# Optimization experiments

Measured on AMD Instinct MI355X. Metric: run time of the kernel, lower is better.

## Reference

```python
import jax, jax.numpy as jnp
import numpy as np

LN_EPS = 1e-3   # keras LayerNormalization default epsilon
STAB = 1e-3     # performer relu-kernel numerical stabilizer
N = 2           # number of blocks per branch


def layer_norm(x, g, b):
    m = jnp.mean(x, axis=-1, keepdims=True)
    v = jnp.mean(jnp.square(x - m), axis=-1, keepdims=True)
    return (x - m) * jax.lax.rsqrt(v + LN_EPS) * g + b


def favor(q_in, kv_in, Wq, Wk, Wv, Wo):
    # Performer FAVOR attention, relu kernel features (google-research fast_attention,
    # projection_matrix_type=None). q/k/v head projections have no bias.
    q = jnp.einsum('bld,dhm->blhm', q_in, Wq)
    k = jnp.einsum('bsd,dhm->bshm', kv_in, Wk)
    v = jnp.einsum('bsd,dhm->bshm', kv_in, Wv)
    norm = q.shape[-1] ** -0.25  # 1/sqrt(sqrt(head_dim))
    qp = jax.nn.relu(q * norm) + STAB
    kp = jax.nn.relu(k * norm) + STAB
    kv = jnp.einsum('bshm,bshd->bhmd', kp, v)
    num = jnp.einsum('blhm,bhmd->blhd', qp, kv)
    den = jnp.einsum('blhm,bhm->blh', qp, kp.sum(axis=1))
    out = num / den[..., None]
    return jnp.einsum('blhd,hde->ble', out, Wo)


def forward(obj_inputs, road_inputs,
            rg_dense_W, rg_dense_b, rg_qkv_W, rg_qkv_b,
            rg_Wq, rg_Wk, rg_Wv, rg_Wo, rg_ln_g, rg_ln_b, rg_fc_W, rg_fc_b,
            rg_out_W, rg_out_b,
            dense_W, dense_b, pos_emb,
            Wq, Wk, Wv, Wo, ln_g, ln_b, fc_W, fc_b):
    rgH = rg_dense_W.shape[1]
    # ---- roadgraph branch: performer self-attention blocks ----
    x = jax.nn.relu(road_inputs @ rg_dense_W + rg_dense_b)
    for i in range(N):
        qkv = jax.nn.relu(x @ rg_qkv_W + rg_qkv_b)
        q = qkv[..., :rgH]  # k,v splits unused by FastSelfAttention (it re-projects q)
        attn = favor(q, q, rg_Wq[i], rg_Wk[i], rg_Wv[i], rg_Wo[i])
        n = layer_norm(attn + x, rg_ln_g[i], rg_ln_b[i])
        y = jax.nn.relu(n @ rg_fc_W[i] + rg_fc_b[i])
        x = layer_norm(n + y, rg_ln_g[i], rg_ln_b[i])  # original reuses ln_block_1
    rg_out = jax.nn.relu(x @ rg_out_W + rg_out_b)
    # ---- object branch: performer cross-attention blocks ----
    x = jax.nn.relu(obj_inputs @ dense_W + dense_b)
    x = x + pos_emb  # learned position embedding, [T, H]
    for i in range(N):
        attn = favor(x, rg_out, Wq[i], Wk[i], Wv[i], Wo[i])
        n = layer_norm(attn + x, ln_g[i], ln_b[i])
        y = jax.nn.relu(n @ fc_W[i] + fc_b[i])
        x = layer_norm(n + y, ln_g[i], ln_b[i])  # original reuses ln_block_1
    return x


def setup_inputs() -> dict:
    B, T, V = 8, 128, 512
    S, F = 8192, 8
    rgH, H = 16, 1024
    rh, rd = 4, 4     # rg heads, head_dim
    h, d = 16, 64     # cross heads, head_dim
    keys = iter(jax.random.split(jax.random.key(0), 64))
    def rnd(shape, scale=1.0):
        return jax.random.normal(next(keys), shape, dtype=jnp.float32) * scale
    return {
        'obj_inputs': rnd((B, T, V)),
        'road_inputs': rnd((B, S, F)),
        'rg_dense_W': rnd((F, rgH), F ** -0.5), 'rg_dense_b': jnp.zeros((rgH,), jnp.float32),
        'rg_qkv_W': rnd((rgH, 3 * rgH), rgH ** -0.5), 'rg_qkv_b': jnp.zeros((3 * rgH,), jnp.float32),
        'rg_Wq': rnd((N, rgH, rh, rd), rgH ** -0.5),
        'rg_Wk': rnd((N, rgH, rh, rd), rgH ** -0.5),
        'rg_Wv': rnd((N, rgH, rh, rd), rgH ** -0.5),
        'rg_Wo': rnd((N, rh, rd, rgH), rgH ** -0.5),
        'rg_ln_g': jnp.ones((N, rgH), jnp.float32), 'rg_ln_b': jnp.zeros((N, rgH), jnp.float32),
        'rg_fc_W': rnd((N, rgH, rgH), rgH ** -0.5), 'rg_fc_b': jnp.zeros((N, rgH), jnp.float32),
        'rg_out_W': rnd((rgH, H), rgH ** -0.5), 'rg_out_b': jnp.zeros((H,), jnp.float32),
        'dense_W': rnd((V, H), V ** -0.5), 'dense_b': jnp.zeros((H,), jnp.float32),
        'pos_emb': rnd((T, H), 0.02),
        'Wq': rnd((N, H, h, d), H ** -0.5),
        'Wk': rnd((N, H, h, d), H ** -0.5),
        'Wv': rnd((N, H, h, d), H ** -0.5),
        'Wo': rnd((N, h, d, H), H ** -0.5),
        'ln_g': jnp.ones((N, H), jnp.float32), 'ln_b': jnp.zeros((N, H), jnp.float32),
        'fc_W': rnd((N, H, H), H ** -0.5), 'fc_b': jnp.zeros((N, H), jnp.float32),
    }


def reference(obj_inputs, road_inputs, rg_dense_W, rg_dense_b, rg_qkv_W, rg_qkv_b,
              rg_Wq, rg_Wk, rg_Wv, rg_Wo, rg_ln_g, rg_ln_b, rg_fc_W, rg_fc_b,
              rg_out_W, rg_out_b, dense_W, dense_b, pos_emb,
              Wq, Wk, Wv, Wo, ln_g, ln_b, fc_W, fc_b):
    return forward(obj_inputs, road_inputs, rg_dense_W, rg_dense_b, rg_qkv_W, rg_qkv_b,
                   rg_Wq, rg_Wk, rg_Wv, rg_Wo, rg_ln_g, rg_ln_b, rg_fc_W, rg_fc_b,
                   rg_out_W, rg_out_b, dense_W, dense_b, pos_emb,
                   Wq, Wk, Wv, Wo, ln_g, ln_b, fc_W, fc_b)
```

## Files before the change

### kernel.cpp

```cpp
#include <hip/hip_runtime.h>

typedef unsigned short u16;
typedef unsigned int u32;

using s8v = __attribute__((ext_vector_type(8))) short;
using f4v = __attribute__((ext_vector_type(4))) float;

#define LN_EPS 0.001f
#define STAB 0.001f
#define NORM_OBJ 0.35355339059327373f
#define NORM_ROAD 0.7071067811865476f

__device__ __forceinline__ float bf2f(u16 v) { return __uint_as_float(((u32)v) << 16); }
__device__ __forceinline__ u16 f2bf(float f) {
  u32 u = __float_as_uint(f);
  u32 r = (u + 0x7fffu + ((u >> 16) & 1u)) >> 16;
  return (u16)r;
}
__device__ __forceinline__ f4v mfma16(s8v a, s8v b, f4v c) {
  return __builtin_amdgcn_mfma_f32_16x16x32_bf16(a, b, c, 0, 0, 0);
}
__device__ __forceinline__ void ldsload16(void* lds, const void* g) {
  __builtin_amdgcn_global_load_lds((const __attribute__((address_space(1))) u32*)g,
                                   (__attribute__((address_space(3))) u32*)lds, 16, 0, 0);
}

struct TPair { const float* s; u16* d; };
struct TP11 { TPair p[11]; };

__global__ __launch_bounds__(256) void transpose_kernel(TP11 ps, int K, int N) {
  const float* __restrict__ src = ps.p[blockIdx.z].s;
  u16* __restrict__ dst = ps.p[blockIdx.z].d;
  int n0 = blockIdx.x * 64, k0 = blockIdx.y * 64;
  int t = threadIdx.x;
  __shared__ __align__(16) u16 lt[64 * 72];
#pragma unroll
  for (int j = 0; j < 4; ++j) {
    int p = t + 256 * j;
    int r = p >> 4, cb = p & 15;
    float4 v = *(const float4*)(src + (size_t)(k0 + r) * N + n0 + cb * 4);
    lt[r * 72 + cb * 4 + 0] = f2bf(v.x);
    lt[r * 72 + cb * 4 + 1] = f2bf(v.y);
    lt[r * 72 + cb * 4 + 2] = f2bf(v.z);
    lt[r * 72 + cb * 4 + 3] = f2bf(v.w);
  }
  __syncthreads();
#pragma unroll
  for (int j = 0; j < 2; ++j) {
    int q = t + 256 * j;
    int on = q >> 3, ocb = q & 7;
    u16 e[8];
#pragma unroll
    for (int i = 0; i < 8; ++i) e[i] = lt[(ocb * 8 + i) * 72 + on];
    uint4 v;
    v.x = (u32)e[0] | ((u32)e[1] << 16);
    v.y = (u32)e[2] | ((u32)e[3] << 16);
    v.z = (u32)e[4] | ((u32)e[5] << 16);
    v.w = (u32)e[6] | ((u32)e[7] << 16);
    *(uint4*)(dst + (size_t)(n0 + on) * K + k0 + ocb * 8) = v;
  }
}

__global__ __launch_bounds__(256) void cvt_kernel(const float* __restrict__ src,
                                                  u16* __restrict__ dst) {
  int i = (blockIdx.x * 256 + threadIdx.x) * 4;
  float4 v = *(const float4*)(src + i);
  uint2 o;
  o.x = (u32)f2bf(v.x) | ((u32)f2bf(v.y) << 16);
  o.y = (u32)f2bf(v.z) | ((u32)f2bf(v.w) << 16);
  *(uint2*)(dst + i) = o;
}

__global__ __launch_bounds__(256) void r0_kernel(const float* __restrict__ road,
    const float* __restrict__ W, const float* __restrict__ bias, float* __restrict__ x) {
  int row = blockIdx.x * 256 + threadIdx.x;
  float in[8];
  float4 v0 = *(const float4*)(road + (size_t)row * 8);
  float4 v1 = *(const float4*)(road + (size_t)row * 8 + 4);
  in[0] = v0.x; in[1] = v0.y; in[2] = v0.z; in[3] = v0.w;
  in[4] = v1.x; in[5] = v1.y; in[6] = v1.z; in[7] = v1.w;
#pragma unroll
  for (int j = 0; j < 16; ++j) {
    float s = bias[j];
#pragma unroll
    for (int c = 0; c < 8; ++c) s += in[c] * W[c * 16 + j];
    x[(size_t)row * 16 + j] = fmaxf(s, 0.f);
  }
}

__global__ __launch_bounds__(256) void ra_kernel(const float* __restrict__ x,
    const float* __restrict__ qkvW, const float* __restrict__ qkvb,
    const float* __restrict__ Wk, const float* __restrict__ Wv,
    float* __restrict__ kvr, float* __restrict__ ksr) {
  int t = threadIdx.x;
  int row = blockIdx.x * 256 + t;
  int b = row >> 13;
  float xv[16];
#pragma unroll
  for (int e = 0; e < 16; ++e) xv[e] = x[(size_t)row * 16 + e];
  float q16[16];
#pragma unroll
  for (int j = 0; j < 16; ++j) {
    float s = qkvb[j];
#pragma unroll
    for (int c = 0; c < 16; ++c) s += xv[c] * qkvW[c * 48 + j];
    q16[j] = fmaxf(s, 0.f);
  }
  float kp[16], vh[16];
#pragma unroll
  for (int hm = 0; hm < 16; ++hm) {
    float sk = 0.f, sv = 0.f;
#pragma unroll
    for (int c = 0; c < 16; ++c) {
      float q = q16[c];
      sk += q * Wk[c * 16 + hm];
      sv += q * Wv[c * 16 + hm];
    }
    kp[hm] = fmaxf(sk * NORM_ROAD, 0.f) + STAB;
    vh[hm] = sv;
  }
  __shared__ float l[80];
  if (t < 80) l[t] = 0.f;
  __syncthreads();
#pragma unroll
  for (int h = 0; h < 4; ++h)
#pragma unroll
    for (int m = 0; m < 4; ++m) {
      float kpv = kp[h * 4 + m];
      atomicAdd(&l[64 + h * 4 + m], kpv);
#pragma unroll
      for (int d = 0; d < 4; ++d) atomicAdd(&l[h * 16 + m * 4 + d], kpv * vh[h * 4 + d]);
    }
  __syncthreads();
  if (t < 64) atomicAdd(&kvr[b * 64 + t], l[t]);
  else if (t < 80) atomicAdd(&ksr[b * 16 + (t - 64)], l[t]);
}

__device__ __forceinline__ void ln16(const float* tv, const float* g, const float* bb, float* o) {
  float m = 0.f;
#pragma unroll
  for (int e = 0; e < 16; ++e) m += tv[e];
  m *= (1.f / 16.f);
  float var = 0.f;
#pragma unroll
  for (int e = 0; e < 16; ++e) { float d = tv[e] - m; var += d * d; }
  var *= (1.f / 16.f);
  float rstd = rsqrtf(var + LN_EPS);
#pragma unroll
  for (int e = 0; e < 16; ++e) o[e] = (tv[e] - m) * rstd * g[e] + bb[e];
}

__global__ __launch_bounds__(256) void rb_kernel(float* __restrict__ x,
    const float* __restrict__ qkvW, const float* __restrict__ qkvb,
    const float* __restrict__ Wq, const float* __restrict__ Wo,
    const float* __restrict__ lng, const float* __restrict__ lnb,
    const float* __restrict__ fcW, const float* __restrict__ fcb,
    const float* __restrict__ kvr, const float* __restrict__ ksr) {
  int row = blockIdx.x * 256 + threadIdx.x;
  int b = row >> 13;
  float xv[16];
#pragma unroll
  for (int e = 0; e < 16; ++e) xv[e] = x[(size_t)row * 16 + e];
  float q16[16];
#pragma unroll
  for (int j = 0; j < 16; ++j) {
    float s = qkvb[j];
#pragma unroll
    for (int c = 0; c < 16; ++c) s += xv[c] * qkvW[c * 48 + j];
    q16[j] = fmaxf(s, 0.f);
  }
  float qp[16];
#pragma unroll
  for (int hm = 0; hm < 16; ++hm) {
    float s = 0.f;
#pragma unroll
    for (int c = 0; c < 16; ++c) s += q16[c] * Wq[c * 16 + hm];
    qp[hm] = fmaxf(s * NORM_ROAD, 0.f) + STAB;
  }
  float attn[16];
#pragma unroll
  for (int e = 0; e < 16; ++e) attn[e] = 0.f;
#pragma unroll
  for (int h = 0; h < 4; ++h) {
    float den = 0.f;
#pragma unroll
    for (int m = 0; m < 4; ++m) den += qp[h * 4 + m] * ksr[b * 16 + h * 4 + m];
    float od[4];
#pragma unroll
    for (int d = 0; d < 4; ++d) {
      float num = 0.f;
#pragma unroll
      for (int m = 0; m < 4; ++m) num += qp[h * 4 + m] * kvr[b * 64 + h * 16 + m * 4 + d];
      od[d] = num / den;
    }
#pragma unroll
    for (int d = 0; d < 4; ++d)
#pragma unroll
      for (int e = 0; e < 16; ++e) attn[e] += od[d] * Wo[(h * 4 + d) * 16 + e];
  }
  float tv[16], n[16], o2[16];
#pragma unroll
  for (int e = 0; e < 16; ++e) tv[e] = attn[e] + xv[e];
  ln16(tv, lng, lnb, n);
#pragma unroll
  for (int j = 0; j < 16; ++j) {
    float s = fcb[j];
#pragma unroll
    for (int e = 0; e < 16; ++e) s += n[e] * fcW[e * 16 + j];
    tv[j] = n[j] + fmaxf(s, 0.f);
  }
  ln16(tv, lng, lnb, o2);
#pragma unroll
  for (int e = 0; e < 16; ++e) x[(size_t)row * 16 + e] = o2[e];
}

__global__ __launch_bounds__(256) void rc_kernel(const float* __restrict__ x,
    const float* __restrict__ W, const float* __restrict__ bias, u16* __restrict__ out) {
  const int t = threadIdx.x;
  const int cg = t & 63, rg = t >> 6;
  const int c0 = blockIdx.x * 256 + cg * 4;
  const int r0 = blockIdx.y * 16;
  __shared__ float lx[256];
  lx[t] = x[(size_t)(r0 + (t >> 4)) * 16 + (t & 15)];
  __syncthreads();
  float4 wv[16];
#pragma unroll
  for (int c = 0; c < 16; ++c) wv[c] = *(const float4*)(W + (size_t)c * 1024 + c0);
  float4 bv = *(const float4*)(bias + c0);
#pragma unroll
  for (int k = 0; k < 4; ++k) {
    int rr = rg * 4 + k;
    float s0 = bv.x, s1 = bv.y, s2 = bv.z, s3 = bv.w;
#pragma unroll
    for (int c = 0; c < 16; ++c) {
      float xv = lx[rr * 16 + c];
      s0 += xv * wv[c].x; s1 += xv * wv[c].y; s2 += xv * wv[c].z; s3 += xv * wv[c].w;
    }
    uint2 o;
    o.x = (u32)f2bf(fmaxf(s0, 0.f)) | ((u32)f2bf(fmaxf(s1, 0.f)) << 16);
    o.y = (u32)f2bf(fmaxf(s2, 0.f)) | ((u32)f2bf(fmaxf(s3, 0.f)) << 16);
    *(uint2*)(out + (size_t)(r0 + rr) * 1024 + c0) = o;
  }
}

__global__ __launch_bounds__(256) void gemm_kernel(
    const u16* __restrict__ A, const u16* __restrict__ BT, int K,
    float* __restrict__ outF, u16* __restrict__ outB,
    const float* __restrict__ bias, const float* __restrict__ resF, int resmod,
    float scale, int do_relu, float post) {
  const int n0 = blockIdx.x * 128, m0 = blockIdx.y * 128;
  const int t = threadIdx.x;
  const int wid = t >> 6, lane = t & 63, quad = lane >> 4, m16 = lane & 15;
  const int wm = wid >> 1, wn = wid & 1;
  const int lrr = lane >> 3;
  const int lcs = (((lane & 7) ^ lrr) * 8);
  const int sw = m16 & 7;
  __shared__ __align__(16) u16 smem[2 * 128 * 64];
  u16* Al = smem;
  u16* Bl = smem + 128 * 64;
  f4v acc[4][4];
#pragma unroll
  for (int i = 0; i < 4; ++i)
#pragma unroll
    for (int j = 0; j < 4; ++j) acc[i][j] = {0.f, 0.f, 0.f, 0.f};

  for (int kc = 0; kc < K; kc += 64) {
    __syncthreads();
#pragma unroll
    for (int j = 0; j < 4; ++j) {
      int rbase = wid * 32 + j * 8;
      ldsload16(Al + rbase * 64, A + (size_t)(m0 + rbase + lrr) * K + kc + lcs);
      ldsload16(Bl + rbase * 64, BT + (size_t)(n0 + rbase + lrr) * K + kc + lcs);
    }
    __syncthreads();
#pragma unroll
    for (int ko = 0; ko < 64; ko += 32) {
      int g0 = ko >> 3;
      s8v af[4], bfr[4];
#pragma unroll
      for (int tm = 0; tm < 4; ++tm)
        af[tm] = *(const s8v*)(Al + (wm * 64 + tm * 16 + m16) * 64 + ((g0 + quad) ^ sw) * 8);
#pragma unroll
      for (int tn = 0; tn < 4; ++tn)
        bfr[tn] = *(const s8v*)(Bl + (wn * 64 + tn * 16 + m16) * 64 + ((g0 + quad) ^ sw) * 8);
#pragma unroll
      for (int tm = 0; tm < 4; ++tm)
#pragma unroll
        for (int tn = 0; tn < 4; ++tn)
          acc[tm][tn] = mfma16(af[tm], bfr[tn], acc[tm][tn]);
    }
  }
#pragma unroll
  for (int tm = 0; tm < 4; ++tm)
#pragma unroll
    for (int tn = 0; tn < 4; ++tn)
#pragma unroll
      for (int r = 0; r < 4; ++r) {
        int row = m0 + wm * 64 + tm * 16 + quad * 4 + r;
        int col = n0 + wn * 64 + tn * 16 + m16;
        float v = acc[tm][tn][r] * scale;
        if (bias) v += bias[col];
        if (do_relu) v = fmaxf(v, 0.f);
        v += post;
        if (resF) v += resF[(size_t)(row % resmod) * 1024 + col];
        if (outF) outF[(size_t)row * 1024 + col] = v;
        if (outB) outB[(size_t)row * 1024 + col] = f2bf(v);
      }
}

__global__ __launch_bounds__(256) void kv_kernel(
    const u16* __restrict__ rgout,
    const u16* __restrict__ WkT0, const u16* __restrict__ WvT0,
    const u16* __restrict__ WkT1, const u16* __restrict__ WvT1,
    float* __restrict__ kv, float* __restrict__ ksum) {
  const int mt = blockIdx.x, h2 = blockIdx.y, b = blockIdx.z;
  const int lay = h2 >> 4, h = h2 & 15;
  const u16* __restrict__ WkT = lay ? WkT1 : WkT0;
  const u16* __restrict__ WvT = lay ? WvT1 : WvT0;
  kv += (size_t)lay * 524288;
  ksum += (size_t)lay * 8192;
  const int t = threadIdx.x;
  const int wid = t >> 6, lane = t & 63, quad = lane >> 4, m16 = lane & 15;
  const int wm = wid >> 1, wn = wid & 1;
  const int lrr = lane >> 3;
  const int lcs = (((lane & 7) ^ lrr) * 8);
  const int sw = m16 & 7;
  __shared__ __align__(16) u16 smem[2 * 128 * 72];
  u16* Al = smem;
  u16* Bl = smem + 128 * 64;
  const size_t abase = ((size_t)b * 8192 + (size_t)mt * 128) * 1024;
  f4v acc[4][4];
#pragma unroll
  for (int i = 0; i < 4; ++i)
#pragma unroll
    for (int j = 0; j < 4; ++j) acc[i][j] = {0.f, 0.f, 0.f, 0.f};

  for (int kc = 0; kc < 1024; kc += 64) {
    __syncthreads();
#pragma unroll
    for (int j = 0; j < 4; ++j) {
      int rbase = wid * 32 + j * 8;
      int r = rbase + lrr;
      ldsload16(Al + rbase * 64, rgout + abase + (size_t)r * 1024 + kc + lcs);
      const u16* bsrc = (r < 64) ? (WkT + (size_t)(h * 64 + r) * 1024)
                                 : (WvT + (size_t)(h * 64 + (r - 64)) * 1024);
      ldsload16(Bl + rbase * 64, bsrc + kc + lcs);
    }
    __syncthreads();
#pragma unroll
    for (int ko = 0; ko < 64; ko += 32) {
      int g0 = ko >> 3;
      s8v af[4], bfr[4];
#pragma unroll
      for (int tm = 0; tm < 4; ++tm)
        af[tm] = *(const s8v*)(Al + (wm * 64 + tm * 16 + m16) * 64 + ((g0 + quad) ^ sw) * 8);
#pragma unroll
      for (int tn = 0; tn < 4; ++tn)
        bfr[tn] = *(const s8v*)(Bl + (wn * 64 + tn * 16 + m16) * 64 + ((g0 + quad) ^ sw) * 8);
#pragma unroll
      for (int tm = 0; tm < 4; ++tm)
#pragma unroll
        for (int tn = 0; tn < 4; ++tn)
          acc[tm][tn] = mfma16(af[tm], bfr[tn], acc[tm][tn]);
    }
  }
  __syncthreads();
  u16* KPT = smem;
  u16* VT = smem + 64 * 136;
  {
    u16* dst = wn ? VT : KPT;
    const int sbase = wm * 64 + quad * 4;
#pragma unroll
    for (int tm = 0; tm < 4; ++tm)
#pragma unroll
      for (int tn = 0; tn < 4; ++tn) {
        float v0 = acc[tm][tn][0], v1 = acc[tm][tn][1];
        float v2 = acc[tm][tn][2], v3 = acc[tm][tn][3];
        if (wn == 0) {
          v0 = fmaxf(v0 * NORM_OBJ, 0.f) + STAB;
          v1 = fmaxf(v1 * NORM_OBJ, 0.f) + STAB;
          v2 = fmaxf(v2 * NORM_OBJ, 0.f) + STAB;
          v3 = fmaxf(v3 * NORM_OBJ, 0.f) + STAB;
        }
        uint2 o;
        o.x = (u32)f2bf(v0) | ((u32)f2bf(v1) << 16);
        o.y = (u32)f2bf(v2) | ((u32)f2bf(v3) << 16);
        int feat = tn * 16 + m16;
        *(uint2*)(dst + feat * 136 + sbase + tm * 16) = o;
      }
  }
  __syncthreads();
  if (t < 64) {
    float s = 0.f;
#pragma unroll
    for (int i = 0; i < 128; i += 8) {
      uint4 v = *(const uint4*)(KPT + t * 136 + i);
      u32 a[4] = {v.x, v.y, v.z, v.w};
#pragma unroll
      for (int q = 0; q < 4; ++q) {
        s += __uint_as_float(a[q] << 16);
        s += __uint_as_float(a[q] & 0xffff0000u);
      }
    }
    atomicAdd(&ksum[(size_t)(b * 16 + h) * 64 + t], s);
  }
  f4v a2[4];
#pragma unroll
  for (int tn = 0; tn < 4; ++tn) a2[tn] = {0.f, 0.f, 0.f, 0.f};
#pragma unroll
  for (int ks = 0; ks < 128; ks += 32) {
    s8v af = *(const s8v*)(KPT + (wid * 16 + m16) * 136 + ks + quad * 8);
#pragma unroll
    for (int tn = 0; tn < 4; ++tn) {
      s8v bv = *(const s8v*)(VT + (tn * 16 + m16) * 136 + ks + quad * 8);
      a2[tn] = mfma16(af, bv, a2[tn]);
    }
  }
#pragma unroll
  for (int tn = 0; tn < 4; ++tn)
#pragma unroll
    for (int r = 0; r < 4; ++r) {
      int m = wid * 16 + quad * 4 + r;
      int d = tn * 16 + m16;
      atomicAdd(&kv[((size_t)(b * 16 + h) * 64 + m) * 64 + d], a2[tn][r]);
    }
}

__global__ __launch_bounds__(256) void q2_kernel(const u16* __restrict__ qp,
    const float* __restrict__ kv, const float* __restrict__ ks, u16* __restrict__ out) {
  int wid = threadIdx.x >> 6, lane = threadIdx.x & 63;
  int row = blockIdx.x * 4 + wid;
  int b = row >> 7;
  int h0 = blockIdx.y * 4;
  for (int h = h0; h < h0 + 4; ++h) {
    const float* kvp = kv + (size_t)((b * 16 + h) * 64) * 64;
    const float* ksp = ks + (size_t)(b * 16 + h) * 64;
    const u16* qpp = qp + (size_t)row * 1024 + h * 64;
    float num = 0.f, den = 0.f;
    for (int m = 0; m < 64; ++m) {
      float qv = bf2f(qpp[m]);
      num += qv * kvp[m * 64 + lane];
      den += qv * ksp[m];
    }
    out[(size_t)row * 1024 + h * 64 + lane] = f2bf(num / den);
  }
}

__global__ __launch_bounds__(256) void ln_kernel(const float* __restrict__ in,
    const float* __restrict__ g, const float* __restrict__ bb,
    float* __restrict__ outF, u16* __restrict__ outB) {
  int row = blockIdx.x, t = threadIdx.x;
  const float* x = in + (size_t)row * 1024;
  float v[4];
  float s = 0.f, ss = 0.f;
#pragma unroll
  for (int j = 0; j < 4; ++j) {
    v[j] = x[t + 256 * j];
    s += v[j];
    ss += v[j] * v[j];
  }
  __shared__ float rs[256], rss[256];
  rs[t] = s; rss[t] = ss;
  __syncthreads();
  for (int o = 128; o > 0; o >>= 1) {
    if (t < o) { rs[t] += rs[t + o]; rss[t] += rss[t + o]; }
    __syncthreads();
  }
  float mean = rs[0] * (1.f / 1024.f);
  float var = rss[0] * (1.f / 1024.f) - mean * mean;
  float rstd = rsqrtf(var + LN_EPS);
#pragma unroll
  for (int j = 0; j < 4; ++j) {
    int c = t + 256 * j;
    float o = (v[j] - mean) * rstd * g[c] + bb[c];
    if (outF) outF[(size_t)row * 1024 + c] = o;
    if (outB) outB[(size_t)row * 1024 + c] = f2bf(o);
  }
}

static constexpr size_t MBy = 1048576;
static constexpr size_t OFF_XROAD = 0;
static constexpr size_t OFF_RGOUT = 4 * MBy;
static constexpr size_t OFF_KVR = OFF_RGOUT + 128 * MBy;
static constexpr size_t OFF_KSR = OFF_KVR + 2048;
static constexpr size_t OFF_KVO = OFF_KVR + 4096;
static constexpr size_t OFF_KSO = OFF_KVO + 4 * MBy;
static constexpr size_t OFF_WT = OFF_KSO + 65536;
static constexpr size_t OFF_XOBJ = OFF_WT + 21 * MBy;
static constexpr size_t OFF_XOBJB = OFF_XOBJ + 4 * MBy;
static constexpr size_t OFF_QP = OFF_XOBJB + 2 * MBy;
static constexpr size_t OFF_FOUT = OFF_QP + 2 * MBy;
static constexpr size_t OFF_T1 = OFF_FOUT + 2 * MBy;
static constexpr size_t OFF_N = OFF_T1 + 4 * MBy;
static constexpr size_t OFF_NB = OFF_N + 4 * MBy;
static constexpr size_t OFF_OBJB = OFF_NB + 2 * MBy;

extern "C" void kernel_launch(void* const* d_in, const int* in_sizes, int n_in,
                              void* d_out, int out_size, void* d_ws, size_t ws_size,
                              hipStream_t stream) {
  (void)in_sizes; (void)n_in; (void)out_size; (void)ws_size;
  const float* obj = (const float*)d_in[0];
  const float* road = (const float*)d_in[1];
  const float* rgdW = (const float*)d_in[2];
  const float* rgdb = (const float*)d_in[3];
  const float* qkvW = (const float*)d_in[4];
  const float* qkvb = (const float*)d_in[5];
  const float* rgWq = (const float*)d_in[6];
  const float* rgWk = (const float*)d_in[7];
  const float* rgWv = (const float*)d_in[8];
  const float* rgWo = (const float*)d_in[9];
  const float* rglng = (const float*)d_in[10];
  const float* rglnb = (const float*)d_in[11];
  const float* rgfcW = (const float*)d_in[12];
  const float* rgfcb = (const float*)d_in[13];
  const float* rgoW = (const float*)d_in[14];
  const float* rgob = (const float*)d_in[15];
  const float* denW = (const float*)d_in[16];
  const float* denb = (const float*)d_in[17];
  const float* pose = (const float*)d_in[18];
  const float* Wq = (const float*)d_in[19];
  const float* Wk = (const float*)d_in[20];
  const float* Wv = (const float*)d_in[21];
  const float* Wo = (const float*)d_in[22];
  const float* lng = (const float*)d_in[23];
  const float* lnb = (const float*)d_in[24];
  const float* fcW = (const float*)d_in[25];
  const float* fcb = (const float*)d_in[26];

  char* w = (char*)d_ws;
  float* xroad = (float*)(w + OFF_XROAD);
  u16* rgout = (u16*)(w + OFF_RGOUT);
  float* kvr = (float*)(w + OFF_KVR);
  float* ksr = (float*)(w + OFF_KSR);
  float* kvo = (float*)(w + OFF_KVO);
  float* kso = (float*)(w + OFF_KSO);
  u16* wt = (u16*)(w + OFF_WT);
  float* xobj = (float*)(w + OFF_XOBJ);
  u16* xobjb = (u16*)(w + OFF_XOBJB);
  u16* qpB = (u16*)(w + OFF_QP);
  u16* fout = (u16*)(w + OFF_FOUT);
  float* t1 = (float*)(w + OFF_T1);
  float* nF = (float*)(w + OFF_N);
  u16* nB = (u16*)(w + OFF_NB);
  u16* objb = (u16*)(w + OFF_OBJB);

  const size_t E = 1048576;
  u16* wqT[2] = {wt + 0 * E, wt + 1 * E};
  u16* wkT[2] = {wt + 2 * E, wt + 3 * E};
  u16* wvT[2] = {wt + 4 * E, wt + 5 * E};
  u16* woT[2] = {wt + 6 * E, wt + 7 * E};
  u16* fcT[2] = {wt + 8 * E, wt + 9 * E};
  u16* denT = wt + 10 * E;

  TP11 tb;
  const float* srcs[10] = {Wq, Wq + E, Wk, Wk + E, Wv, Wv + E, Wo, Wo + E, fcW, fcW + E};
  u16* dsts[10] = {wqT[0], wqT[1], wkT[0], wkT[1], wvT[0], wvT[1], woT[0], woT[1], fcT[0], fcT[1]};
  for (int j = 0; j < 11; ++j) { tb.p[j].s = srcs[j < 10 ? j : 0]; tb.p[j].d = dsts[j < 10 ? j : 0]; }
  transpose_kernel<<<dim3(16, 16, 10), 256, 0, stream>>>(tb, 1024, 1024);
  TP11 td;
  for (int j = 0; j < 11; ++j) { td.p[j].s = denW; td.p[j].d = denT; }
  transpose_kernel<<<dim3(16, 8, 1), 256, 0, stream>>>(td, 512, 1024);
  cvt_kernel<<<dim3(512), 256, 0, stream>>>(obj, objb);

  r0_kernel<<<dim3(256), 256, 0, stream>>>(road, rgdW, rgdb, xroad);
  for (int i = 0; i < 2; ++i) {
    hipMemsetAsync(w + OFF_KVR, 0, 2560, stream);
    ra_kernel<<<dim3(256), 256, 0, stream>>>(xroad, qkvW, qkvb, rgWk + i * 256, rgWv + i * 256,
                                             kvr, ksr);
    rb_kernel<<<dim3(256), 256, 0, stream>>>(xroad, qkvW, qkvb, rgWq + i * 256, rgWo + i * 256,
                                             rglng + i * 16, rglnb + i * 16, rgfcW + i * 256,
                                             rgfcb + i * 16, kvr, ksr);
  }
  rc_kernel<<<dim3(4, 4096), 256, 0, stream>>>(xroad, rgoW, rgob, rgout);

  hipMemsetAsync(w + OFF_KVO, 0, 4 * MBy + 65536, stream);
  kv_kernel<<<dim3(64, 32, 8), 256, 0, stream>>>(rgout, wkT[0], wvT[0], wkT[1], wvT[1], kvo, kso);

  gemm_kernel<<<dim3(8, 8), 256, 0, stream>>>(objb, denT, 512, xobj, xobjb, denb, pose, 128,
                                              1.f, 1, 0.f);

  for (int i = 0; i < 2; ++i) {
    gemm_kernel<<<dim3(8, 8), 256, 0, stream>>>(xobjb, wqT[i], 1024, nullptr, qpB, nullptr,
                                                nullptr, 1024, NORM_OBJ, 1, STAB);
    q2_kernel<<<dim3(256, 4), 256, 0, stream>>>(qpB, kvo + (size_t)i * 524288,
                                                kso + (size_t)i * 8192, fout);
    gemm_kernel<<<dim3(8, 8), 256, 0, stream>>>(fout, woT[i], 1024, t1, nullptr, nullptr, xobj,
                                                1024, 1.f, 0, 0.f);
    ln_kernel<<<dim3(1024), 256, 0, stream>>>(t1, lng + i * 1024, lnb + i * 1024, nF, nB);
    gemm_kernel<<<dim3(8, 8), 256, 0, stream>>>(nB, fcT[i], 1024, t1, nullptr, fcb + i * 1024, nF,
                                                1024, 1.f, 1, 0.f);
    if (i == 0)
      ln_kernel<<<dim3(1024), 256, 0, stream>>>(t1, lng, lnb, xobj, xobjb);
    else
      ln_kernel<<<dim3(1024), 256, 0, stream>>>(t1, lng + 1024, lnb + 1024, (float*)d_out, nullptr);
  }
}
```

Measured before the change: 1.668 ms.

## Process two heads per kv_kernel block to reuse the road-output tile

The K/V projection kernel now computes two heads per block using 512 threads and a 128x256 output tile instead of 128x128. Each staged tile of road-output rows is reused across both heads, which halves global and LDS-fill traffic for the large activation operand. The grid's head dimension is halved to match. In exchange, each block uses more LDS (about 68 KB for the epilogue staging) and has twice as many waves, which can lower resident blocks per CU and the number of blocks available to fill the GPU.

```diff
diff --git a/kernel.cpp b/kernel.cpp
--- a/kernel.cpp
+++ b/kernel.cpp
@@ -308,24 +308,25 @@
       }
 }
 
-__global__ __launch_bounds__(256) void kv_kernel(
+__global__ __launch_bounds__(512) void kv_kernel(
     const u16* __restrict__ rgout,
     const u16* __restrict__ WkT0, const u16* __restrict__ WvT0,
     const u16* __restrict__ WkT1, const u16* __restrict__ WvT1,
     float* __restrict__ kv, float* __restrict__ ksum) {
-  const int mt = blockIdx.x, h2 = blockIdx.y, b = blockIdx.z;
-  const int lay = h2 >> 4, h = h2 & 15;
+  const int mt = blockIdx.x, y = blockIdx.y, b = blockIdx.z;
+  const int lay = y >> 3, hp = y & 7;
   const u16* __restrict__ WkT = lay ? WkT1 : WkT0;
   const u16* __restrict__ WvT = lay ? WvT1 : WvT0;
   kv += (size_t)lay * 524288;
   ksum += (size_t)lay * 8192;
   const int t = threadIdx.x;
   const int wid = t >> 6, lane = t & 63, quad = lane >> 4, m16 = lane & 15;
-  const int wm = wid >> 1, wn = wid & 1;
+  const int wm = wid >> 2, wn = wid & 3;
   const int lrr = lane >> 3;
   const int lcs = (((lane & 7) ^ lrr) * 8);
   const int sw = m16 & 7;
-  __shared__ __align__(16) u16 smem[2 * 128 * 72];
+  const int HSZ = 64 * 136;
+  __shared__ __align__(16) u16 smem[4 * 64 * 136];
   u16* Al = smem;
   u16* Bl = smem + 128 * 64;
   const size_t abase = ((size_t)b * 8192 + (size_t)mt * 128) * 1024;
@@ -338,12 +339,17 @@
   for (int kc = 0; kc < 1024; kc += 64) {
     __syncthreads();
 #pragma unroll
+    for (int j = 0; j < 2; ++j) {
+      int rbase = wid * 16 + j * 8;
+      ldsload16(Al + rbase * 64, rgout + abase + (size_t)(rbase + lrr) * 1024 + kc + lcs);
+    }
+#pragma unroll
     for (int j = 0; j < 4; ++j) {
       int rbase = wid * 32 + j * 8;
       int r = rbase + lrr;
-      ldsload16(Al + rbase * 64, rgout + abase + (size_t)r * 1024 + kc + lcs);
-      const u16* bsrc = (r < 64) ? (WkT + (size_t)(h * 64 + r) * 1024)
-                                 : (WvT + (size_t)(h * 64 + (r - 64)) * 1024);
+      int h = hp * 2 + (r >> 7), rr = r & 127;
+      const u16* bsrc = (rr < 64) ? (WkT + (size_t)(h * 64 + rr) * 1024)
+                                  : (WvT + (size_t)(h * 64 + (rr - 64)) * 1024);
       ldsload16(Bl + rbase * 64, bsrc + kc + lcs);
     }
     __syncthreads();
@@ -365,10 +371,10 @@
     }
   }
   __syncthreads();
-  u16* KPT = smem;
-  u16* VT = smem + 64 * 136;
   {
-    u16* dst = wn ? VT : KPT;
+    int hh = wn >> 1;
+    u16* dst = smem + (size_t)(hh * 2 + (wn & 1)) * HSZ;
+    const int iskp = (wn & 1) == 0;
     const int sbase = wm * 64 + quad * 4;
 #pragma unroll
     for (int tm = 0; tm < 4; ++tm)
@@ -376,7 +382,7 @@
       for (int tn = 0; tn < 4; ++tn) {
         float v0 = acc[tm][tn][0], v1 = acc[tm][tn][1];
         float v2 = acc[tm][tn][2], v3 = acc[tm][tn][3];
-        if (wn == 0) {
+        if (iskp) {
           v0 = fmaxf(v0 * NORM_OBJ, 0.f) + STAB;
           v1 = fmaxf(v1 * NORM_OBJ, 0.f) + STAB;
           v2 = fmaxf(v2 * NORM_OBJ, 0.f) + STAB;
@@ -390,11 +396,13 @@
       }
   }
   __syncthreads();
-  if (t < 64) {
+  if (t < 128) {
+    int hh = t >> 6, m = t & 63;
+    const u16* base = smem + (size_t)(hh * 2) * HSZ + m * 136;
     float s = 0.f;
 #pragma unroll
     for (int i = 0; i < 128; i += 8) {
-      uint4 v = *(const uint4*)(KPT + t * 136 + i);
+      uint4 v = *(const uint4*)(base + i);
       u32 a[4] = {v.x, v.y, v.z, v.w};
 #pragma unroll
       for (int q = 0; q < 4; ++q) {
@@ -402,28 +410,34 @@
         s += __uint_as_float(a[q] & 0xffff0000u);
       }
     }
-    atomicAdd(&ksum[(size_t)(b * 16 + h) * 64 + t], s);
-  }
-  f4v a2[4];
-#pragma unroll
-  for (int tn = 0; tn < 4; ++tn) a2[tn] = {0.f, 0.f, 0.f, 0.f};
-#pragma unroll
-  for (int ks = 0; ks < 128; ks += 32) {
-    s8v af = *(const s8v*)(KPT + (wid * 16 + m16) * 136 + ks + quad * 8);
-#pragma unroll
-    for (int tn = 0; tn < 4; ++tn) {
-      s8v bv = *(const s8v*)(VT + (tn * 16 + m16) * 136 + ks + quad * 8);
-      a2[tn] = mfma16(af, bv, a2[tn]);
-    }
-  }
-#pragma unroll
-  for (int tn = 0; tn < 4; ++tn)
-#pragma unroll
-    for (int r = 0; r < 4; ++r) {
-      int m = wid * 16 + quad * 4 + r;
-      int d = tn * 16 + m16;
-      atomicAdd(&kv[((size_t)(b * 16 + h) * 64 + m) * 64 + d], a2[tn][r]);
-    }
+    atomicAdd(&ksum[(size_t)(b * 16 + hp * 2 + hh) * 64 + m], s);
+  }
+  {
+    int hh = wid >> 2, mq = wid & 3;
+    const u16* KPh = smem + (size_t)(hh * 2) * HSZ;
+    const u16* Vh = KPh + HSZ;
+    f4v a2[4];
+#pragma unroll
+    for (int tn = 0; tn < 4; ++tn) a2[tn] = {0.f, 0.f, 0.f, 0.f};
+#pragma unroll
+    for (int ks = 0; ks < 128; ks += 32) {
+      s8v af = *(const s8v*)(KPh + (mq * 16 + m16) * 136 + ks + quad * 8);
+#pragma unroll
+      for (int tn = 0; tn < 4; ++tn) {
+        s8v bv = *(const s8v*)(Vh + (tn * 16 + m16) * 136 + ks + quad * 8);
+        a2[tn] = mfma16(af, bv, a2[tn]);
+      }
+    }
+    int h = hp * 2 + hh;
+#pragma unroll
+    for (int tn = 0; tn < 4; ++tn)
+#pragma unroll
+      for (int r = 0; r < 4; ++r) {
+        int m = mq * 16 + quad * 4 + r;
+        int d = tn * 16 + m16;
+        atomicAdd(&kv[((size_t)(b * 16 + h) * 64 + m) * 64 + d], a2[tn][r]);
+      }
+  }
 }
 
 __global__ __launch_bounds__(256) void q2_kernel(const u16* __restrict__ qp,
@@ -574,7 +588,7 @@
   rc_kernel<<<dim3(4, 4096), 256, 0, stream>>>(xroad, rgoW, rgob, rgout);
 
   hipMemsetAsync(w + OFF_KVO, 0, 4 * MBy + 65536, stream);
-  kv_kernel<<<dim3(64, 32, 8), 256, 0, stream>>>(rgout, wkT[0], wvT[0], wkT[1], wvT[1], kvo, kso);
+  kv_kernel<<<dim3(64, 16, 8), 512, 0, stream>>>(rgout, wkT[0], wvT[0], wkT[1], wvT[1], kvo, kso);
 
   gemm_kernel<<<dim3(8, 8), 256, 0, stream>>>(objb, denT, 512, xobj, xobjb, denb, pose, 128,
                                               1.f, 1, 0.f);
```

New measurement: 1.484 ms. -11.1%, faster.
